# Performance work log

Hardware: AMD Instinct MI355X
Metric: run time of the kernel (lower is better)

## Reference

```python
import jax, jax.numpy as jnp
import numpy as np


def _shared_mlp(x, W, s, b):
    # 1x1 conv over channel dim (last axis) + folded BN (scale/shift) + ReLU
    # x: (..., Cin), W: (Cout, Cin), s/b: (Cout,)
    return jax.nn.relu(jnp.einsum('...c,oc->...o', x, W) * s + b)


def setup_inputs() -> dict:
    key = jax.random.key(0)
    ks = jax.random.split(key, 15)
    B, N, K, C = 4, 4096, 32, 64
    D1, D2, DH = 64, 64, 128
    sc = 0.1
    return {
        'xyz': jax.random.normal(ks[0], (B, N, 3), dtype=jnp.float32),
        'features': jax.random.normal(ks[1], (B, C, N), dtype=jnp.float32),
        'idx': jax.random.randint(ks[2], (N, K), 0, N, dtype=jnp.int32),
        'W_gu': jax.random.normal(ks[3], (D1, 6), dtype=jnp.float32) * sc,
        's_gu': jnp.ones((D1,), jnp.float32),
        'b_gu': jax.random.normal(ks[4], (D1,), dtype=jnp.float32) * sc,
        'W_gv': jax.random.normal(ks[5], (D2, C), dtype=jnp.float32) * sc,
        's_gv': jnp.ones((D2,), jnp.float32),
        'b_gv': jax.random.normal(ks[6], (D2,), dtype=jnp.float32) * sc,
        'W_h': jax.random.normal(ks[7], (DH, D1 + D2), dtype=jnp.float32) * sc,
        's_h': jnp.ones((DH,), jnp.float32),
        'b_h': jax.random.normal(ks[8], (DH,), dtype=jnp.float32) * sc,
        'W_f': jax.random.normal(ks[9], (C, DH), dtype=jnp.float32) * sc,
        's_f': jnp.ones((C,), jnp.float32),
        'b_f': jax.random.normal(ks[10], (C,), dtype=jnp.float32) * sc,
    }


def reference(xyz, features, idx, W_gu, s_gu, b_gu, W_gv, s_gv, b_gv,
              W_h, s_h, b_h, W_f, s_f, b_f):
    # xyz: (B,N,3), features: (B,C,N), idx: (N,K) neighbor indices per point
    feats = jnp.swapaxes(features, 1, 2)              # (B,N,C)
    xyz_nb = xyz[:, idx, :]                           # (B,N,K,3) random gather
    feat_nb = feats[:, idx, :]                        # (B,N,K,C)
    K = idx.shape[1]
    center_xyz = jnp.broadcast_to(xyz[:, :, None, :], xyz_nb.shape)
    rel_xyz = jnp.concatenate([center_xyz, xyz_nb], axis=-1)   # (B,N,K,6)
    rel_feat = feat_nb + feats[:, :, None, :]                  # (B,N,K,C)

    gu = _shared_mlp(rel_xyz, W_gu, s_gu, b_gu)       # (B,N,K,D1)
    gv = _shared_mlp(rel_feat, W_gv, s_gv, b_gv)      # (B,N,K,D2)
    fuse = jnp.concatenate([gu, gv], axis=-1)         # (B,N,K,D1+D2)
    h = _shared_mlp(fuse, W_h, s_h, b_h)              # (B,N,K,DH)
    pooled = jnp.mean(h, axis=2)                      # (B,N,DH) mean over K
    out = _shared_mlp(pooled, W_f, s_f, b_f)          # (B,N,C)
    out = jnp.swapaxes(out, 1, 2) + features          # (B,C,N) residual
    return (xyz, out)
```

## Files before the change

kernel.cpp:

```cpp
#include <hip/hip_runtime.h>

#define B_  4
#define N_  4096
#define K_  32
#define C_  64
#define DH_ 128
#define PPW 8

typedef _Float16 half2v __attribute__((ext_vector_type(2)));
typedef _Float16 half8  __attribute__((ext_vector_type(8)));
typedef __fp16   fp16x2 __attribute__((ext_vector_type(2)));
typedef float  floatx16 __attribute__((ext_vector_type(16)));
typedef unsigned int uint_t;

union HU { half2v h; uint_t u; };
union HU2 { fp16x2 h; uint_t u; };

__device__ __forceinline__ uint_t pk2(float a, float b) {
    HU2 x; x.h = __builtin_amdgcn_cvt_pkrtz(a, b);
    return x.u;
}

__global__ __launch_bounds__(256) void k_prep(
    const float* __restrict__ xyz,
    const float* __restrict__ features,
    const float* __restrict__ W_gv,
    const float* __restrict__ W_gu,
    const float* __restrict__ s_gu, const float* __restrict__ b_gu,
    const float* __restrict__ s_gv, const float* __restrict__ b_gv,
    const float* __restrict__ W_h,  const float* __restrict__ s_h,
    float* __restrict__ out_xyz,
    _Float16* __restrict__ Bpack,
    uint_t* __restrict__ QsH,
    uint_t* __restrict__ PcatH)
{
    const int blk = blockIdx.x;
    const int b   = blk >> 8;
    const int n0  = (blk & 255) * 16;
    const int t   = threadIdx.x;

    if (t < 48) { int e = blk*48 + t; out_xyz[e] = xyz[e]; }
    if (t >= 64 && t < 80) {
        int e = blk*16 + (t - 64);
        int j = e & 7, l = (e >> 3) & 63, c = (e >> 9) & 7, ob = e >> 12;
        int o = ob*32 + (l & 31);
        int i = c*16 + (l >> 5)*8 + j;
        Bpack[e] = (_Float16)(W_h[o*DH_ + i] * s_h[o]);
    }

    __shared__ __align__(16) float ftile[64 * 17];
    __shared__ __align__(16) float wtile[64 * 68];

    {
        const int c = t >> 2, nq = t & 3;
        const float4 f4 = *(const float4*)&features[(b*C_ + c)*N_ + n0 + nq*4];
        ftile[c*17 + nq*4 + 0] = f4.x;
        ftile[c*17 + nq*4 + 1] = f4.y;
        ftile[c*17 + nq*4 + 2] = f4.z;
        ftile[c*17 + nq*4 + 3] = f4.w;
    }
#pragma unroll
    for (int r = 0; r < 4; r++) {
        const int e4 = r*256 + t, o = e4 >> 4, c0 = (e4 & 15)*4;
        const float4 w4 = *(const float4*)&W_gv[o*C_ + c0];
        wtile[(c0+0)*68 + o] = w4.x;
        wtile[(c0+1)*68 + o] = w4.y;
        wtile[(c0+2)*68 + o] = w4.z;
        wtile[(c0+3)*68 + o] = w4.w;
    }
    __syncthreads();

    const int n  = t >> 4;
    const int oq = t & 15;
    const int o0 = oq * 4;

    float acc[4] = {};
#pragma unroll 4
    for (int c = 0; c < 64; c++) {
        const float a = ftile[c*17 + n];
        const float4 wv = *(const float4*)&wtile[c*68 + o0];
        acc[0] = fmaf(a, wv.x, acc[0]);
        acc[1] = fmaf(a, wv.y, acc[1]);
        acc[2] = fmaf(a, wv.z, acc[2]);
        acc[3] = fmaf(a, wv.w, acc[3]);
    }

    const int bn = b*N_ + n0 + n;
    const float x0 = xyz[bn*3+0], x1 = xyz[bn*3+1], x2 = xyz[bn*3+2];

    const float4 sgu = *(const float4*)&s_gu[o0];
    const float4 bgu = *(const float4*)&b_gu[o0];
    const float4 sgv = *(const float4*)&s_gv[o0];
    const float4 bgv = *(const float4*)&b_gv[o0];

    float q[4], r[4];
#pragma unroll
    for (int jj = 0; jj < 4; jj++) {
        const int o = o0 + jj;
        q[jj] = x0*W_gu[o*6+0] + x1*W_gu[o*6+1] + x2*W_gu[o*6+2];
        r[jj] = x0*W_gu[o*6+3] + x1*W_gu[o*6+4] + x2*W_gu[o*6+5];
    }
    uint2 qa, pa;
    qa.x = pk2(q[0]*sgu.x+bgu.x, q[1]*sgu.y+bgu.y);
    qa.y = pk2(q[2]*sgu.z+bgu.z, q[3]*sgu.w+bgu.w);
    pa.x = pk2(r[0]*sgu.x, r[1]*sgu.y);
    pa.y = pk2(r[2]*sgu.z, r[3]*sgu.w);
    *(uint2*)&QsH  [bn*64 + oq*2] = qa;
    *(uint2*)&PcatH[bn*64 + oq*2] = pa;
    qa.x = pk2(acc[0]*sgv.x+bgv.x, acc[1]*sgv.y+bgv.y);
    qa.y = pk2(acc[2]*sgv.z+bgv.z, acc[3]*sgv.w+bgv.w);
    pa.x = pk2(acc[0]*sgv.x, acc[1]*sgv.y);
    pa.y = pk2(acc[2]*sgv.z, acc[3]*sgv.w);
    *(uint2*)&QsH  [bn*64 + 32 + oq*2] = qa;
    *(uint2*)&PcatH[bn*64 + 32 + oq*2] = pa;
}

__global__ __launch_bounds__(128) void k_main(
    const int*      __restrict__ idx,
    const uint_t*   __restrict__ QsH,
    const uint_t*   __restrict__ PcatH,
    const _Float16* __restrict__ Bpack,
    const float*    __restrict__ b_h,
    float* __restrict__ Pool)
{
    const int t    = threadIdx.x;
    const int ohu  = __builtin_amdgcn_readfirstlane(t >> 6);
    const int lane = t & 63;
    const int m    = lane & 31;
    const int hh   = lane >> 5;

    __shared__ uint_t fuse[2][32 * 66];

    half8 Bf[2][8];
#pragma unroll
    for (int ob = 0; ob < 2; ob++)
#pragma unroll
        for (int c = 0; c < 8; c++)
            Bf[ob][c] = *(const half8*)&Bpack[(((ohu*2 + ob)*8 + c)*64 + lane)*8];

    const float bh0  = b_h[(ohu*2+0)*32 + m];
    const float bh1  = b_h[(ohu*2+1)*32 + m];
    const float nbh0 = -bh0, nbh1 = -bh1;
    const float b32_0 = 32.f * bh0, b32_1 = 32.f * bh1;

    const int bnb   = blockIdx.x * PPW;
    const int base0 = bnb & ~(N_ - 1);

    uint_t pg[16];
    uint_t qw;
    int js[16];

    {
        const int n0p = bnb & (N_ - 1);
        const int* ip = idx + n0p*K_ + ohu*16;
#pragma unroll
        for (int it = 0; it < 16; it++) js[it] = ip[it];
        qw = QsH[(size_t)bnb*64 + lane];
#pragma unroll
        for (int it = 0; it < 16; it++)
            pg[it] = PcatH[((size_t)(base0 + js[it]) << 6) + lane];
#pragma unroll
        for (int it = 0; it < 16; it++) {
            HU a, pval; a.u = qw; pval.u = pg[it];
            half2v v = a.h + pval.h;
            HU o2; o2.h = __builtin_elementwise_max(v, (half2v){(_Float16)0.f,(_Float16)0.f});
            fuse[0][(ohu*16 + it)*66 + lane] = o2.u;
        }
    }
    __syncthreads();

#pragma unroll
    for (int p = 0; p < PPW; p++) {
        const int cur = p & 1, nxt = cur ^ 1;

        uint_t qw_n = 0;
        if (p + 1 < PPW) {
            const int np = (bnb + p + 1) & (N_ - 1);
            const int* ip = idx + np*K_ + ohu*16;
#pragma unroll
            for (int it = 0; it < 16; it++) js[it] = ip[it];
            qw_n = QsH[(size_t)(bnb + p + 1)*64 + lane];
#pragma unroll
            for (int it = 0; it < 16; it++)
                pg[it] = PcatH[((size_t)(base0 + js[it]) << 6) + lane];
        }

        floatx16 acc0 = {}, acc1 = {};
#pragma unroll
        for (int c = 0; c < 8; c++) {
            const int wb = m*66 + c*8 + hh*4;
            union { uint_t u[4]; half8 h; } av;
            *(uint2*)&av.u[0] = *(const uint2*)&fuse[cur][wb];
            *(uint2*)&av.u[2] = *(const uint2*)&fuse[cur][wb + 2];
            acc0 = __builtin_amdgcn_mfma_f32_32x32x16_f16(av.h, Bf[0][c], acc0, 0, 0, 0);
            acc1 = __builtin_amdgcn_mfma_f32_32x32x16_f16(av.h, Bf[1][c], acc1, 0, 0, 0);
        }
        float v0 = 0.f, v1 = 0.f;
#pragma unroll
        for (int rg = 0; rg < 16; rg++) {
            v0 += fmaxf(acc0[rg], nbh0);
            v1 += fmaxf(acc1[rg], nbh1);
        }
        v0 += __shfl_xor(v0, 32);
        v1 += __shfl_xor(v1, 32);
        if (hh == 0) {
            Pool[(size_t)(bnb + p)*128 + (ohu*2+0)*32 + m] = v0 + b32_0;
            Pool[(size_t)(bnb + p)*128 + (ohu*2+1)*32 + m] = v1 + b32_1;
        }

        if (p + 1 < PPW) {
#pragma unroll
            for (int it = 0; it < 16; it++) {
                HU a, pval; a.u = qw_n; pval.u = pg[it];
                half2v v = a.h + pval.h;
                HU o2; o2.h = __builtin_elementwise_max(v, (half2v){(_Float16)0.f,(_Float16)0.f});
                fuse[nxt][(ohu*16 + it)*66 + lane] = o2.u;
            }
        }
        __syncthreads();
    }
}

__global__ __launch_bounds__(256) void k_post(
    const float* __restrict__ Pool,
    const float* __restrict__ W_f,
    const float* __restrict__ s_f, const float* __restrict__ b_f,
    const float* __restrict__ features,
    float* __restrict__ outF)
{
    const int b   = blockIdx.x >> 8;
    const int n0  = (blockIdx.x & 255) * 16;
    const int t   = threadIdx.x;
    const int bn0 = b*N_ + n0;

    __shared__ __align__(16) float pt[16 * 132];
    __shared__ __align__(16) float wt[128 * 68];
    __shared__ float ot[64 * 17];

    for (int e = t; e < 16*128; e += 256) {
        const int nl = e >> 7, i = e & 127;
        pt[nl*132 + i] = Pool[(size_t)(bn0 + nl)*128 + i];
    }
    for (int e = t; e < C_*DH_; e += 256) {
        const int c = e >> 7, i = e & 127;
        wt[i*68 + c] = W_f[e];
    }
    __syncthreads();

    const int nl = t >> 4;
    const int cq = t & 15;
    const int c0 = cq * 4;

    float acc[4] = {};
#pragma unroll 4
    for (int i = 0; i < DH_; i++) {
        const float p = pt[nl*132 + i];
        const float4 wv = *(const float4*)&wt[i*68 + c0];
        acc[0] = fmaf(p, wv.x, acc[0]);
        acc[1] = fmaf(p, wv.y, acc[1]);
        acc[2] = fmaf(p, wv.z, acc[2]);
        acc[3] = fmaf(p, wv.w, acc[3]);
    }
    const float4 sf = *(const float4*)&s_f[c0];
    const float4 bf = *(const float4*)&b_f[c0];
    const float inv_k = 1.f / (float)K_;
    ot[(c0+0)*17 + nl] = fmaxf(acc[0]*inv_k*sf.x + bf.x, 0.f);
    ot[(c0+1)*17 + nl] = fmaxf(acc[1]*inv_k*sf.y + bf.y, 0.f);
    ot[(c0+2)*17 + nl] = fmaxf(acc[2]*inv_k*sf.z + bf.z, 0.f);
    ot[(c0+3)*17 + nl] = fmaxf(acc[3]*inv_k*sf.w + bf.w, 0.f);
    __syncthreads();

    {
        const int c = t >> 2, nq = t & 3;
        const float4 fr = *(const float4*)&features[(b*C_ + c)*N_ + n0 + nq*4];
        float4 ov;
        ov.x = ot[c*17 + nq*4 + 0] + fr.x;
        ov.y = ot[c*17 + nq*4 + 1] + fr.y;
        ov.z = ot[c*17 + nq*4 + 2] + fr.z;
        ov.w = ot[c*17 + nq*4 + 3] + fr.w;
        *(float4*)&outF[(b*C_ + c)*N_ + n0 + nq*4] = ov;
    }
}

extern "C" void kernel_launch(void* const* d_in, const int* in_sizes, int n_in,
                              void* d_out, int out_size, void* d_ws, size_t ws_size,
                              hipStream_t stream)
{
    const float* xyz      = (const float*)d_in[0];
    const float* features = (const float*)d_in[1];
    const int*   idx      = (const int*)  d_in[2];
    const float* W_gu     = (const float*)d_in[3];
    const float* s_gu     = (const float*)d_in[4];
    const float* b_gu     = (const float*)d_in[5];
    const float* W_gv     = (const float*)d_in[6];
    const float* s_gv     = (const float*)d_in[7];
    const float* b_gv     = (const float*)d_in[8];
    const float* W_h      = (const float*)d_in[9];
    const float* s_h      = (const float*)d_in[10];
    const float* b_h      = (const float*)d_in[11];
    const float* W_f      = (const float*)d_in[12];
    const float* s_f      = (const float*)d_in[13];
    const float* b_f      = (const float*)d_in[14];

    float* out  = (float*)d_out;
    float* outF = out + B_*N_*3;

    char* wp = (char*)d_ws;
    uint_t*   QsH   = (uint_t*)wp;   wp += (size_t)B_*N_*64*4;
    uint_t*   PcatH = (uint_t*)wp;   wp += (size_t)B_*N_*64*4;
    float*    Pool  = (float*)wp;    wp += (size_t)B_*N_*128*4;
    _Float16* Bpack = (_Float16*)wp; wp += DH_*DH_*2;

    k_prep<<<B_*(N_/16), 256, 0, stream>>>(xyz, features, W_gv, W_gu,
                                           s_gu, b_gu, s_gv, b_gv, W_h, s_h,
                                           out, Bpack, QsH, PcatH);
    k_main<<<(B_*N_)/PPW, 128, 0, stream>>>(idx, QsH, PcatH, Bpack, b_h, Pool);
    k_post<<<B_*(N_/16), 256, 0, stream>>>(Pool, W_f, s_f, b_f, features, outF);
}
```

Measured before the change: 132.6 us.

## Restructure k_main to single-wave blocks computing all 128 outputs per point

k_main now runs one 64-lane wave per block. That wave gathers all 32 neighbours for a point and issues four MFMA output tiles, so the work is no longer split across two waves. Because one wave owns the whole fuse tile, the double-buffered shared memory and the __syncthreads barriers are removed, and points per block drop from 8 to 4. The trade-off is higher register pressure: the wave holds 32 B-fragment vectors, 32 gathered values and four accumulators, which could limit occupancy. With a single wave, gather latency is also hidden only within that wave.

```diff
diff --git a/kernel.cpp b/kernel.cpp
--- a/kernel.cpp
+++ b/kernel.cpp
@@ -5,7 +5,7 @@
 #define K_  32
 #define C_  64
 #define DH_ 128
-#define PPW 8
+#define PPW 4
 
 typedef _Float16 half2v __attribute__((ext_vector_type(2)));
 typedef _Float16 half8  __attribute__((ext_vector_type(8)));
@@ -115,7 +115,7 @@
     *(uint2*)&PcatH[bn*64 + 32 + oq*2] = pa;
 }
 
-__global__ __launch_bounds__(128) void k_main(
+__global__ __launch_bounds__(64, 2) void k_main(
     const int*      __restrict__ idx,
     const uint_t*   __restrict__ QsH,
     const uint_t*   __restrict__ PcatH,
@@ -123,101 +123,107 @@
     const float*    __restrict__ b_h,
     float* __restrict__ Pool)
 {
-    const int t    = threadIdx.x;
-    const int ohu  = __builtin_amdgcn_readfirstlane(t >> 6);
-    const int lane = t & 63;
+    const int lane = threadIdx.x;
     const int m    = lane & 31;
     const int hh   = lane >> 5;
 
-    __shared__ uint_t fuse[2][32 * 66];
-
-    half8 Bf[2][8];
-#pragma unroll
-    for (int ob = 0; ob < 2; ob++)
+    __shared__ uint_t fuse[32 * 66];
+
+    half8 Bf[4][8];
+#pragma unroll
+    for (int ob = 0; ob < 4; ob++)
 #pragma unroll
         for (int c = 0; c < 8; c++)
-            Bf[ob][c] = *(const half8*)&Bpack[(((ohu*2 + ob)*8 + c)*64 + lane)*8];
-
-    const float bh0  = b_h[(ohu*2+0)*32 + m];
-    const float bh1  = b_h[(ohu*2+1)*32 + m];
-    const float nbh0 = -bh0, nbh1 = -bh1;
-    const float b32_0 = 32.f * bh0, b32_1 = 32.f * bh1;
+            Bf[ob][c] = *(const half8*)&Bpack[((ob*8 + c)*64 + lane)*8];
+
+    float nbh[4], b32[4];
+#pragma unroll
+    for (int ob = 0; ob < 4; ob++) {
+        const float bh = b_h[ob*32 + m];
+        nbh[ob] = -bh;
+        b32[ob] = 32.f * bh;
+    }
 
     const int bnb   = blockIdx.x * PPW;
     const int base0 = bnb & ~(N_ - 1);
 
-    uint_t pg[16];
+    uint_t pg[32];
     uint_t qw;
-    int js[16];
 
     {
-        const int n0p = bnb & (N_ - 1);
-        const int* ip = idx + n0p*K_ + ohu*16;
-#pragma unroll
-        for (int it = 0; it < 16; it++) js[it] = ip[it];
+        const int* ip = idx + (bnb & (N_-1))*K_;
+        int js[32];
+#pragma unroll
+        for (int it = 0; it < 32; it++) js[it] = ip[it];
         qw = QsH[(size_t)bnb*64 + lane];
 #pragma unroll
-        for (int it = 0; it < 16; it++)
+        for (int it = 0; it < 32; it++)
             pg[it] = PcatH[((size_t)(base0 + js[it]) << 6) + lane];
 #pragma unroll
-        for (int it = 0; it < 16; it++) {
-            HU a, pval; a.u = qw; pval.u = pg[it];
-            half2v v = a.h + pval.h;
+        for (int it = 0; it < 32; it++) {
+            HU a, pv; a.u = qw; pv.u = pg[it];
+            half2v v = a.h + pv.h;
             HU o2; o2.h = __builtin_elementwise_max(v, (half2v){(_Float16)0.f,(_Float16)0.f});
-            fuse[0][(ohu*16 + it)*66 + lane] = o2.u;
-        }
-    }
-    __syncthreads();
+            fuse[it*66 + lane] = o2.u;
+        }
+    }
 
 #pragma unroll
     for (int p = 0; p < PPW; p++) {
-        const int cur = p & 1, nxt = cur ^ 1;
-
         uint_t qw_n = 0;
         if (p + 1 < PPW) {
-            const int np = (bnb + p + 1) & (N_ - 1);
-            const int* ip = idx + np*K_ + ohu*16;
-#pragma unroll
-            for (int it = 0; it < 16; it++) js[it] = ip[it];
+            const int* ip = idx + ((bnb + p + 1) & (N_-1))*K_;
+            int js[32];
+#pragma unroll
+            for (int it = 0; it < 32; it++) js[it] = ip[it];
             qw_n = QsH[(size_t)(bnb + p + 1)*64 + lane];
 #pragma unroll
-            for (int it = 0; it < 16; it++)
+            for (int it = 0; it < 32; it++)
                 pg[it] = PcatH[((size_t)(base0 + js[it]) << 6) + lane];
         }
 
-        floatx16 acc0 = {}, acc1 = {};
+        floatx16 acc0 = {}, acc1 = {}, acc2 = {}, acc3 = {};
 #pragma unroll
         for (int c = 0; c < 8; c++) {
             const int wb = m*66 + c*8 + hh*4;
             union { uint_t u[4]; half8 h; } av;
-            *(uint2*)&av.u[0] = *(const uint2*)&fuse[cur][wb];
-            *(uint2*)&av.u[2] = *(const uint2*)&fuse[cur][wb + 2];
+            *(uint2*)&av.u[0] = *(const uint2*)&fuse[wb];
+            *(uint2*)&av.u[2] = *(const uint2*)&fuse[wb + 2];
             acc0 = __builtin_amdgcn_mfma_f32_32x32x16_f16(av.h, Bf[0][c], acc0, 0, 0, 0);
             acc1 = __builtin_amdgcn_mfma_f32_32x32x16_f16(av.h, Bf[1][c], acc1, 0, 0, 0);
-        }
-        float v0 = 0.f, v1 = 0.f;
+            acc2 = __builtin_amdgcn_mfma_f32_32x32x16_f16(av.h, Bf[2][c], acc2, 0, 0, 0);
+            acc3 = __builtin_amdgcn_mfma_f32_32x32x16_f16(av.h, Bf[3][c], acc3, 0, 0, 0);
+        }
+
+        float v0 = 0.f, v1 = 0.f, v2 = 0.f, v3 = 0.f;
 #pragma unroll
         for (int rg = 0; rg < 16; rg++) {
-            v0 += fmaxf(acc0[rg], nbh0);
-            v1 += fmaxf(acc1[rg], nbh1);
+            v0 += fmaxf(acc0[rg], nbh[0]);
+            v1 += fmaxf(acc1[rg], nbh[1]);
+            v2 += fmaxf(acc2[rg], nbh[2]);
+            v3 += fmaxf(acc3[rg], nbh[3]);
         }
         v0 += __shfl_xor(v0, 32);
         v1 += __shfl_xor(v1, 32);
+        v2 += __shfl_xor(v2, 32);
+        v3 += __shfl_xor(v3, 32);
         if (hh == 0) {
-            Pool[(size_t)(bnb + p)*128 + (ohu*2+0)*32 + m] = v0 + b32_0;
-            Pool[(size_t)(bnb + p)*128 + (ohu*2+1)*32 + m] = v1 + b32_1;
+            float* pp = Pool + (size_t)(bnb + p)*128;
+            pp[ 0 + m] = v0 + b32[0];
+            pp[32 + m] = v1 + b32[1];
+            pp[64 + m] = v2 + b32[2];
+            pp[96 + m] = v3 + b32[3];
         }
 
         if (p + 1 < PPW) {
 #pragma unroll
-            for (int it = 0; it < 16; it++) {
-                HU a, pval; a.u = qw_n; pval.u = pg[it];
-                half2v v = a.h + pval.h;
+            for (int it = 0; it < 32; it++) {
+                HU a, pv; a.u = qw_n; pv.u = pg[it];
+                half2v v = a.h + pv.h;
                 HU o2; o2.h = __builtin_elementwise_max(v, (half2v){(_Float16)0.f,(_Float16)0.f});
-                fuse[nxt][(ohu*16 + it)*66 + lane] = o2.u;
+                fuse[it*66 + lane] = o2.u;
             }
         }
-        __syncthreads();
     }
 }
 
@@ -314,6 +320,6 @@
     k_prep<<<B_*(N_/16), 256, 0, stream>>>(xyz, features, W_gv, W_gu,
                                            s_gu, b_gu, s_gv, b_gv, W_h, s_h,
                                            out, Bpack, QsH, PcatH);
-    k_main<<<(B_*N_)/PPW, 128, 0, stream>>>(idx, QsH, PcatH, Bpack, b_h, Pool);
+    k_main<<<(B_*N_)/PPW, 64, 0, stream>>>(idx, QsH, PcatH, Bpack, b_h, Pool);
     k_post<<<B_*(N_/16), 256, 0, stream>>>(Pool, W_f, s_f, b_f, features, outF);
 }
```

New measurement: 131.9 us. Within noise of the previous version (-0.5%).
